# Kernel tuning notes

Hardware: AMD Instinct MI355X
Metric: run time of the kernel (lower is better)

## Reference

```python
import jax, jax.numpy as jnp
import numpy as np


def setup_inputs() -> dict:
    key = jax.random.key(0)
    k1, k2, k3, k4 = jax.random.split(key, 4)
    d_in, d_out = 1024, 1024
    x = jax.random.normal(k1, (4, 2048, d_in), dtype=jnp.float32)
    # nn.Linear weights, stored as [d_in, d_out] for x @ W (torch stores transpose)
    s = 1.0 / np.sqrt(d_in)
    Wq = jax.random.normal(k2, (d_in, d_out), dtype=jnp.float32) * s
    Wk = jax.random.normal(k3, (d_in, d_out), dtype=jnp.float32) * s
    Wv = jax.random.normal(k4, (d_in, d_out), dtype=jnp.float32) * s
    return {"x": x, "Wq": Wq, "Wk": Wk, "Wv": Wv}


def reference(x, Wq, Wk, Wv):
    # x: [b, s, d_in]; projections (no bias)
    q = jnp.einsum('bsi,io->bso', x, Wq)
    k = jnp.einsum('bsi,io->bso', x, Wk)
    v = jnp.einsum('bsi,io->bso', x, Wv)
    d_out = k.shape[-1]
    scores = jnp.einsum('bqd,bkd->bqk', q, k) / jnp.sqrt(jnp.float32(d_out))
    seq_len = x.shape[1]
    causal = jnp.tril(jnp.ones((seq_len, seq_len), dtype=bool))  # [s, s]
    scores = jnp.where(causal[None, :, :], scores, -jnp.inf)
    weights = jax.nn.softmax(scores, axis=-1)
    return jnp.einsum('bqk,bkd->bqd', weights, v)
```

## Files before the change

### kernel.cpp

```cpp
#include <hip/hip_runtime.h>

typedef __attribute__((ext_vector_type(8))) short bf16x8;
typedef __attribute__((ext_vector_type(4))) float f32x4;
typedef unsigned int u32;

__device__ __forceinline__ unsigned short f2bf(float f) {
  union { float f; unsigned int u; } a; a.f = f;
  unsigned int u = a.u;
  u += 0x7FFFu + ((u >> 16) & 1u);
  return (unsigned short)(u >> 16);
}

__device__ __forceinline__ void gload16(const unsigned short* g, unsigned short* l) {
  __builtin_amdgcn_global_load_lds((const __attribute__((address_space(1))) u32*)g,
                                   (__attribute__((address_space(3))) u32*)l, 16, 0, 0);
}

#define BK 64

template<int MODE>
__global__ __launch_bounds__(256, 4)
void gemm_bt(const unsigned short* __restrict__ A,
             const unsigned short* __restrict__ Bm,
             float* __restrict__ Cf,
             float* __restrict__ Cf2,
             unsigned short* __restrict__ Cb,
             int K, long aBatch, long bBatch, long cBatch, float scale)
{
  constexpr int NI    = (MODE == 0) ? 4 : 2;
  constexpr int TNc   = (MODE == 0) ? 128 : 64;
  constexpr int BROWS = (MODE == 0) ? 32 : 16;
  constexpr int BG    = (MODE == 0) ? 4 : 2;

  int z = blockIdx.z;
  A  += (long)z * aBatch;
  Bm += (long)z * bBatch;
  if (MODE == 2) { Cb += (long)z * cBatch; Cf += (long)z * 2048; }
  if (MODE == 3) { Cf += (long)z * cBatch; Cf2 += (long)z * 2048; }

  int bm0 = 0, bn, p = 0;
  if (MODE == 2) {
    int f = blockIdx.x;
    int r = (int)((sqrtf((float)(4 * f + 1)) - 1.0f) * 0.5f);
    while ((r + 1) * (r + 2) <= f) r++;
    while (r * (r + 1) > f) r--;
    bm0 = r * 128;
    bn  = (f - r * (r + 1)) * 64;
  } else if (MODE == 3) {
    p  = blockIdx.y;
    bn = blockIdx.x * 64;
  } else {
    bm0 = blockIdx.y * 128;
    bn  = blockIdx.x * 128;
  }

  __shared__ __align__(16) unsigned short As[128 * BK];
  __shared__ __align__(16) unsigned short Bs[TNc * BK];

  int tid  = threadIdx.x;
  int wave = tid >> 6, lane = tid & 63;
  int wm = (MODE == 0) ? (wave >> 1) * 64 : wave * 32;
  int wn = (MODE == 0) ? (wave & 1) * 64 : 0;
  int quad = lane >> 4, l16 = lane & 15;

  int r8 = lane >> 3;
  int c  = (lane & 7) ^ r8;
  const unsigned short* Bg = Bm + (long)(bn + wave * BROWS + r8) * K + c * 8;
  unsigned short* Al = &As[(wave * 32) * BK];
  unsigned short* Bl = &Bs[(wave * BROWS) * BK];

  const int nseg = (MODE == 3) ? 2 : 1;
  for (int seg = 0; seg < nseg; seg++) {
    int bm   = (MODE == 3) ? ((seg == 0) ? (15 - p) * 128 : p * 128) : bm0;
    int Keff = (MODE == 3) ? ((seg == 0) ? 128 * (16 - p) : 128 * (p + 1)) : K;
    const unsigned short* Ag = A + (long)(bm + wave * 32 + r8) * K + c * 8;

    f32x4 acc[NI][4] = {};

    for (int k0 = 0; k0 < Keff; k0 += BK) {
#pragma unroll
      for (int g = 0; g < 4; g++)
        gload16(Ag + k0 + (long)g * 8 * K, Al + g * 8 * BK);
#pragma unroll
      for (int g = 0; g < BG; g++)
        gload16(Bg + k0 + (long)g * 8 * K, Bl + g * 8 * BK);
      __syncthreads();

#pragma unroll
      for (int h = 0; h < 2; h++) {
        bf16x8 af[NI], bfr[4];
#pragma unroll
        for (int i = 0; i < NI; i++)
          af[i]  = *(const bf16x8*)&As[(wm + i * 16 + l16) * BK + (((quad + 4 * h) ^ (l16 & 7)) * 8)];
#pragma unroll
        for (int j = 0; j < 4; j++)
          bfr[j] = *(const bf16x8*)&Bs[(wn + j * 16 + l16) * BK + (((quad + 4 * h) ^ (l16 & 7)) * 8)];
#pragma unroll
        for (int i = 0; i < NI; i++)
#pragma unroll
          for (int j = 0; j < 4; j++)
            acc[i][j] = __builtin_amdgcn_mfma_f32_16x16x32_bf16(af[i], bfr[j], acc[i][j], 0, 0, 0);
      }
      __syncthreads();
    }

#pragma unroll
    for (int i = 0; i < NI; i++) {
      int grow0 = bm + wm + i * 16 + quad * 4;
      if (MODE == 2) {
#pragma unroll
        for (int r = 0; r < 4; r++) {
          int grow = grow0 + r;
          float rowpart = 0.f;
#pragma unroll
          for (int j = 0; j < 4; j++) {
            int gcol = bn + j * 16 + l16;
            float e = (gcol <= grow) ? __expf(acc[i][j][r] * scale) : 0.f;
            rowpart += e;
            Cb[(long)grow * 2048 + gcol] = f2bf(e);
          }
          rowpart += __shfl_xor(rowpart, 1);
          rowpart += __shfl_xor(rowpart, 2);
          rowpart += __shfl_xor(rowpart, 4);
          rowpart += __shfl_xor(rowpart, 8);
          if (l16 == 0) atomicAdd(&Cf[grow], rowpart);
        }
      } else if (MODE == 3) {
        float rinv[4];
#pragma unroll
        for (int r = 0; r < 4; r++) rinv[r] = 1.0f / Cf2[grow0 + r];
#pragma unroll
        for (int j = 0; j < 4; j++) {
          int gcol = bn + j * 16 + l16;
#pragma unroll
          for (int r = 0; r < 4; r++)
            Cf[(long)(grow0 + r) * 1024 + gcol] = acc[i][j][r] * rinv[r];
        }
      } else {
#pragma unroll
        for (int j = 0; j < 4; j++) {
          int gcol = bn + wn + j * 16 + l16;
          int which = gcol >> 10;
          int col = gcol & 1023;
          if (which < 2) {
            unsigned short* dst = Cb + (long)which * 8192 * 1024;
#pragma unroll
            for (int r = 0; r < 4; r++)
              dst[(long)(grow0 + r) * 1024 + col] = f2bf(acc[i][j][r]);
          } else {
            unsigned short* Vt = Cb + (long)2 * 8192 * 1024;
            int bb = grow0 >> 11, s = grow0 & 2047;
            ushort4 pk;
            pk.x = f2bf(acc[i][j][0]); pk.y = f2bf(acc[i][j][1]);
            pk.z = f2bf(acc[i][j][2]); pk.w = f2bf(acc[i][j][3]);
            *(ushort4*)(Vt + ((long)bb * 1024 + col) * 2048 + s) = pk;
          }
        }
      }
    }
  }
}

__global__ __launch_bounds__(256)
void prep(const float* __restrict__ x,
          const float* __restrict__ W0, const float* __restrict__ W1,
          const float* __restrict__ W2,
          unsigned short* __restrict__ Xb,
          unsigned short* __restrict__ T0, unsigned short* __restrict__ T1,
          unsigned short* __restrict__ T2,
          float* __restrict__ rsum)
{
  __shared__ float tile[32][33];
  int b = blockIdx.x;
  if (b < 8192) {
    long i = ((long)b * 256 + threadIdx.x) * 4;
    float4 v = *(const float4*)(x + i);
    ushort4 o;
    o.x = f2bf(v.x); o.y = f2bf(v.y); o.z = f2bf(v.z); o.w = f2bf(v.w);
    *(ushort4*)(Xb + i) = o;
  } else if (b < 11264) {
    int t = b - 8192;
    int z = t >> 10, q = t & 1023;
    const float* W    = (z == 0) ? W0 : (z == 1) ? W1 : W2;
    unsigned short* T = (z == 0) ? T0 : (z == 1) ? T1 : T2;
    int kb = (q >> 5) * 32, nb = (q & 31) * 32;
    int tx = threadIdx.x & 31, ty = threadIdx.x >> 5;
    for (int r = ty; r < 32; r += 8)
      tile[r][tx] = W[(long)(kb + r) * 1024 + nb + tx];
    __syncthreads();
    for (int r = ty; r < 32; r += 8)
      T[(long)(nb + r) * 1024 + kb + tx] = f2bf(tile[tx][r]);
  } else {
    long i = ((long)(b - 11264) * 256 + threadIdx.x) * 4;
    float4 zz = {0.f, 0.f, 0.f, 0.f};
    *(float4*)(rsum + i) = zz;
  }
}

extern "C" void kernel_launch(void* const* d_in, const int* in_sizes, int n_in,
                              void* d_out, int out_size, void* d_ws, size_t ws_size,
                              hipStream_t stream) {
  const float* x  = (const float*)d_in[0];
  const float* Wq = (const float*)d_in[1];
  const float* Wk = (const float*)d_in[2];
  const float* Wv = (const float*)d_in[3];
  float* out = (float*)d_out;

  unsigned short* Xb  = (unsigned short*)d_ws;
  unsigned short* WqT = Xb  + (long)8192 * 1024;
  unsigned short* Q   = WqT + (long)3072 * 1024;
  unsigned short* Kb  = Q   + (long)8192 * 1024;
  unsigned short* Vt  = Kb  + (long)8192 * 1024;
  unsigned short* E   = Vt  + (long)8192 * 1024;
  float* rsum         = (float*)(E + (long)4 * 2048 * 2048);
  unsigned short* WkT = WqT + (long)1024 * 1024;
  unsigned short* WvT = WkT + (long)1024 * 1024;

  prep<<<11272, 256, 0, stream>>>(x, Wq, Wk, Wv, Xb, WqT, WkT, WvT, rsum);

  gemm_bt<0><<<dim3(24, 64, 1), 256, 0, stream>>>(Xb, WqT, nullptr, nullptr, Q,
      1024, 0, 0, 0, 1.f);

  gemm_bt<2><<<dim3(272, 1, 4), 256, 0, stream>>>(Q, Kb, rsum, nullptr, E, 1024,
      (long)2048 * 1024, (long)2048 * 1024, (long)2048 * 2048, 0.03125f);

  gemm_bt<3><<<dim3(16, 8, 4), 256, 0, stream>>>(E, Vt, out, rsum, nullptr, 2048,
      (long)2048 * 2048, (long)1024 * 2048, (long)2048 * 1024, 1.f);
}
```

Before: 223.5 us.

## Fold Wq·Wkᵀ into one matrix so scores use x directly instead of K

Rewrites the scores as (x·Wq·Wkᵀ)·xᵀ. A small GEMM first builds M = Wq·Wkᵀ in bf16. The projection GEMM then produces T = x·M and Vᵀ, which is 2048 output columns instead of 3072. The score GEMM uses T and the bf16 x as B, so the separate K projection is dropped. This saves about a third of the projection FLOPs for the cost of a 1024³ GEMM. It also adds an extra bf16 rounding of M, which could affect accuracy.

```diff
diff --git a/kernel.cpp b/kernel.cpp
--- a/kernel.cpp
+++ b/kernel.cpp
@@ -51,7 +51,7 @@
     bn = blockIdx.x * 64;
   } else {
     bm0 = blockIdx.y * 128;
-    bn  = blockIdx.x * 128;
+    bn  = blockIdx.x * TNc;
   }
 
   __shared__ __align__(16) unsigned short As[128 * BK];
@@ -136,19 +136,26 @@
           for (int r = 0; r < 4; r++)
             Cf[(long)(grow0 + r) * 1024 + gcol] = acc[i][j][r] * rinv[r];
         }
+      } else if (MODE == 1) {
+#pragma unroll
+        for (int j = 0; j < 4; j++) {
+          int gcol = bn + j * 16 + l16;
+#pragma unroll
+          for (int r = 0; r < 4; r++)
+            Cb[(long)(grow0 + r) * 1024 + gcol] = f2bf(acc[i][j][r]);
+        }
       } else {
 #pragma unroll
         for (int j = 0; j < 4; j++) {
           int gcol = bn + wn + j * 16 + l16;
           int which = gcol >> 10;
           int col = gcol & 1023;
-          if (which < 2) {
-            unsigned short* dst = Cb + (long)which * 8192 * 1024;
+          if (which == 0) {
 #pragma unroll
             for (int r = 0; r < 4; r++)
-              dst[(long)(grow0 + r) * 1024 + col] = f2bf(acc[i][j][r]);
+              Cb[(long)(grow0 + r) * 1024 + col] = f2bf(acc[i][j][r]);
           } else {
-            unsigned short* Vt = Cb + (long)2 * 8192 * 1024;
+            unsigned short* Vt = Cb + (long)8192 * 1024;
             int bb = grow0 >> 11, s = grow0 & 2047;
             ushort4 pk;
             pk.x = f2bf(acc[i][j][0]); pk.y = f2bf(acc[i][j][1]);
@@ -166,8 +173,8 @@
           const float* __restrict__ W0, const float* __restrict__ W1,
           const float* __restrict__ W2,
           unsigned short* __restrict__ Xb,
-          unsigned short* __restrict__ T0, unsigned short* __restrict__ T1,
-          unsigned short* __restrict__ T2,
+          unsigned short* __restrict__ Wqb, unsigned short* __restrict__ Wkb,
+          unsigned short* __restrict__ WvT,
           float* __restrict__ rsum)
 {
   __shared__ float tile[32][33];
@@ -178,18 +185,24 @@
     ushort4 o;
     o.x = f2bf(v.x); o.y = f2bf(v.y); o.z = f2bf(v.z); o.w = f2bf(v.w);
     *(ushort4*)(Xb + i) = o;
+  } else if (b < 10240) {
+    int t = b - 8192;
+    const float* W    = (t < 1024) ? W0 : W1;
+    unsigned short* D = (t < 1024) ? Wqb : Wkb;
+    long i = ((long)(t & 1023) * 256 + threadIdx.x) * 4;
+    float4 v = *(const float4*)(W + i);
+    ushort4 o;
+    o.x = f2bf(v.x); o.y = f2bf(v.y); o.z = f2bf(v.z); o.w = f2bf(v.w);
+    *(ushort4*)(D + i) = o;
   } else if (b < 11264) {
-    int t = b - 8192;
-    int z = t >> 10, q = t & 1023;
-    const float* W    = (z == 0) ? W0 : (z == 1) ? W1 : W2;
-    unsigned short* T = (z == 0) ? T0 : (z == 1) ? T1 : T2;
+    int q = b - 10240;
     int kb = (q >> 5) * 32, nb = (q & 31) * 32;
     int tx = threadIdx.x & 31, ty = threadIdx.x >> 5;
     for (int r = ty; r < 32; r += 8)
-      tile[r][tx] = W[(long)(kb + r) * 1024 + nb + tx];
+      tile[r][tx] = W2[(long)(kb + r) * 1024 + nb + tx];
     __syncthreads();
     for (int r = ty; r < 32; r += 8)
-      T[(long)(nb + r) * 1024 + kb + tx] = f2bf(tile[tx][r]);
+      WvT[(long)(nb + r) * 1024 + kb + tx] = f2bf(tile[tx][r]);
   } else {
     long i = ((long)(b - 11264) * 256 + threadIdx.x) * 4;
     float4 zz = {0.f, 0.f, 0.f, 0.f};
@@ -207,21 +220,24 @@
   float* out = (float*)d_out;
 
   unsigned short* Xb  = (unsigned short*)d_ws;
-  unsigned short* WqT = Xb  + (long)8192 * 1024;
-  unsigned short* Q   = WqT + (long)3072 * 1024;
-  unsigned short* Kb  = Q   + (long)8192 * 1024;
-  unsigned short* Vt  = Kb  + (long)8192 * 1024;
+  unsigned short* Wqb = Xb  + (long)8192 * 1024;
+  unsigned short* Wkb = Wqb + (long)1024 * 1024;
+  unsigned short* TVB = Wkb + (long)1024 * 1024;
+  unsigned short* T   = TVB + (long)2048 * 1024;
+  unsigned short* Vt  = T   + (long)8192 * 1024;
   unsigned short* E   = Vt  + (long)8192 * 1024;
   float* rsum         = (float*)(E + (long)4 * 2048 * 2048);
-  unsigned short* WkT = WqT + (long)1024 * 1024;
-  unsigned short* WvT = WkT + (long)1024 * 1024;
-
-  prep<<<11272, 256, 0, stream>>>(x, Wq, Wk, Wv, Xb, WqT, WkT, WvT, rsum);
-
-  gemm_bt<0><<<dim3(24, 64, 1), 256, 0, stream>>>(Xb, WqT, nullptr, nullptr, Q,
+
+  prep<<<11272, 256, 0, stream>>>(x, Wq, Wk, Wv, Xb, Wqb, Wkb,
+                                  TVB + (long)1024 * 1024, rsum);
+
+  gemm_bt<1><<<dim3(16, 8, 1), 256, 0, stream>>>(Wkb, Wqb, nullptr, nullptr, TVB,
       1024, 0, 0, 0, 1.f);
 
-  gemm_bt<2><<<dim3(272, 1, 4), 256, 0, stream>>>(Q, Kb, rsum, nullptr, E, 1024,
+  gemm_bt<0><<<dim3(16, 64, 1), 256, 0, stream>>>(Xb, TVB, nullptr, nullptr, T,
+      1024, 0, 0, 0, 1.f);
+
+  gemm_bt<2><<<dim3(272, 1, 4), 256, 0, stream>>>(T, Xb, rsum, nullptr, E, 1024,
       (long)2048 * 1024, (long)2048 * 1024, (long)2048 * 2048, 0.03125f);
 
   gemm_bt<3><<<dim3(16, 8, 4), 256, 0, stream>>>(E, Vt, out, rsum, nullptr, 2048,
```

New measurement: 222.6 us. No clear change (-0.4%).
